# Kernel tuning notes

Hardware: AMD Instinct MI355X
Metric: run time of the kernel (lower is better)

The kernel has to match this reference:

```python
import jax, jax.numpy as jnp
import numpy as np

D = 1024       # d_model
S = 32         # n_slots
EMA = 0.05     # slot_ema (alpha)
RSCALE = 1.0   # read_logit_scale
LN_EPS = 1e-5


def setup_inputs() -> dict:
    key = jax.random.key(0)
    ks = jax.random.split(key, 6)
    B, T = 2, 2048
    h = jax.random.normal(ks[0], (B, T, D), jnp.float32)
    # init_batched_memory_state: small random slots
    state0 = jax.random.normal(ks[1], (B, S, D), jnp.float32) * 0.01
    # xavier_uniform for (out=D, in=D) Linear weights, zero bias
    bound = float(np.sqrt(6.0 / (D + D)))
    Wq = jax.random.uniform(ks[2], (D, D), jnp.float32, -bound, bound)
    Wv = jax.random.uniform(ks[3], (D, D), jnp.float32, -bound, bound)
    bq = jnp.zeros((D,), jnp.float32)
    bv = jnp.zeros((D,), jnp.float32)
    ln_gamma = jnp.ones((D,), jnp.float32)
    ln_beta = jnp.zeros((D,), jnp.float32)
    return {"h": h, "state0": state0, "ln_gamma": ln_gamma, "ln_beta": ln_beta,
            "Wq": Wq, "bq": bq, "Wv": Wv, "bv": bv, "chunk_size": 128}


def _layer_norm(x, gamma, beta):
    mu = jnp.mean(x, axis=-1, keepdims=True)
    var = jnp.mean(jnp.square(x - mu), axis=-1, keepdims=True)
    return (x - mu) * jax.lax.rsqrt(var + LN_EPS) * gamma + beta


def reference(h, state0, ln_gamma, ln_beta, Wq, bq, Wv, bv, chunk_size):
    """write_parallel (soft-routed EMA prefix-scan write) followed by
    read_parallel (per-token softmax slot attention). Returns (ctx, final_state)."""
    B, T, d = h.shape
    alpha = EMA
    a = 1.0 - alpha
    h_norm = _layer_norm(h, ln_gamma, ln_beta)                  # (B,T,d)
    v = h_norm @ Wv.T + bv                                      # value_proj
    q = h_norm @ Wq.T + bq                                      # query_proj
    scale = RSCALE * d ** (-0.5)
    # routing weights from queries vs initial state (breaks seq dependency)
    scores = jnp.einsum('btd,bsd->bts', q, state0) * scale       # (B,T,S)
    w = jax.nn.softmax(scores, axis=-1)
    u = alpha * w[..., None] * v[:, :, None, :]                  # (B,T,S,d)

    n_chunks = T // chunk_size
    Cn = chunk_size
    u_chunks = u.reshape(B, n_chunks, Cn, S, d).transpose(1, 0, 2, 3, 4)
    t_idx = jnp.arange(Cn, dtype=h.dtype)
    decay = a ** t_idx                                           # (Cn,)
    inv_decay = 1.0 / jnp.clip(decay, 1e-30)
    t1_decay = a ** (t_idx + 1.0)

    def step(state, u_c):  # state (B,S,d), u_c (B,Cn,S,d)
        cs = jnp.cumsum(u_c * inv_decay[None, :, None, None], axis=1)
        chunk_states = (decay[None, :, None, None] * cs
                        + t1_decay[None, :, None, None] * state[:, None])
        return chunk_states[:, -1], chunk_states

    final_state, states = jax.lax.scan(step, state0, u_chunks)
    states = states.transpose(1, 0, 2, 3, 4).reshape(B, T, S, d)  # (B,T,S,d)

    # read_parallel: softmax slot attention per token against its own state
    scores_r = jnp.einsum('btd,btsd->bts', q, states) * scale
    attn = jax.nn.softmax(scores_r, axis=-1)
    ctx = jnp.einsum('bts,btsd->btd', attn, states)               # (B,T,d)
    return ctx, final_state
```

## Files before the change

### kernel.cpp

```cpp
#include <hip/hip_runtime.h>

#define Bn 2
#define Tn 2048
#define Dn 1024
#define Sn 32
#define CH 64
#define NCH 32
#define ALPHA 0.05f
#define Adec 0.95f
#define SCALE 0.03125f

typedef __attribute__((ext_vector_type(8))) __bf16 bf16x8;
typedef __attribute__((ext_vector_type(4))) __bf16 bf16x4;
typedef __attribute__((ext_vector_type(4))) float f32x4;

__device__ __forceinline__ void async_copy16(const void* g, void* l) {
  __builtin_amdgcn_global_load_lds(
      (const __attribute__((address_space(1))) unsigned int*)g,
      (__attribute__((address_space(3))) unsigned int*)l, 16, 0, 0);
}

__device__ __forceinline__ bool is_bf16(const void* gam) {
  return ((const unsigned short*)gam)[0] == 0x3F80u;
}

#define W8 (Dn * Dn / 8)
#define S8 (Bn * Sn * Dn / 8)
#define LNB (Bn * Tn)
__global__ __launch_bounds__(256) void prep_k(
    const void* __restrict__ hp, const void* __restrict__ gp, const void* __restrict__ bp,
    const void* __restrict__ Wq, const void* __restrict__ Wv, const void* __restrict__ s0,
    __bf16* __restrict__ hn, __bf16* __restrict__ Wqb, __bf16* __restrict__ Wvb,
    __bf16* __restrict__ s0b) {
  bool isb = is_bf16(gp);
  int tid = threadIdx.x;
  if (blockIdx.x >= LNB) {
    int g = (blockIdx.x - LNB) * 256 + tid;
    const void* src; __bf16* dst; int off;
    if (g < W8)            { src = Wq; dst = Wqb; off = g; }
    else if (g < 2 * W8)   { src = Wv; dst = Wvb; off = g - W8; }
    else                   { src = s0; dst = s0b; off = g - 2 * W8; }
    if (isb) {
      *(bf16x8*)&dst[(size_t)off * 8] = ((const bf16x8*)src)[off];
    } else {
      const float* s = (const float*)src + (size_t)off * 8;
      f32x4 a = *(const f32x4*)s, b = *(const f32x4*)(s + 4);
      bf16x8 t;
      t[0] = (__bf16)a[0]; t[1] = (__bf16)a[1]; t[2] = (__bf16)a[2]; t[3] = (__bf16)a[3];
      t[4] = (__bf16)b[0]; t[5] = (__bf16)b[1]; t[6] = (__bf16)b[2]; t[7] = (__bf16)b[3];
      *(bf16x8*)&dst[(size_t)off * 8] = t;
    }
    return;
  }
  int row = blockIdx.x;
  float x0, x1, x2, x3;
  if (isb) {
    const __bf16* x = (const __bf16*)hp + (size_t)row * Dn;
    bf16x4 xv = *(const bf16x4*)&x[tid * 4];
    x0 = (float)xv[0]; x1 = (float)xv[1]; x2 = (float)xv[2]; x3 = (float)xv[3];
  } else {
    const float* x = (const float*)hp + (size_t)row * Dn;
    f32x4 xv = *(const f32x4*)&x[tid * 4];
    x0 = xv[0]; x1 = xv[1]; x2 = xv[2]; x3 = xv[3];
  }
  float s  = x0 + x1 + x2 + x3;
  float s2 = x0*x0 + x1*x1 + x2*x2 + x3*x3;
  #pragma unroll
  for (int m = 32; m >= 1; m >>= 1) { s += __shfl_xor(s, m); s2 += __shfl_xor(s2, m); }
  __shared__ float red[8];
  int wave = tid >> 6, lane = tid & 63;
  if (lane == 0) { red[wave] = s; red[4 + wave] = s2; }
  __syncthreads();
  s  = red[0] + red[1] + red[2] + red[3];
  s2 = red[4] + red[5] + red[6] + red[7];
  float mu  = s * (1.0f / Dn);
  float var = s2 * (1.0f / Dn) - mu * mu;
  float rs  = rsqrtf(var + 1e-5f);
  float g0, g1, g2, g3, be0, be1, be2, be3;
  if (isb) {
    bf16x4 gv = *(const bf16x4*)&((const __bf16*)gp)[tid * 4];
    bf16x4 bv = *(const bf16x4*)&((const __bf16*)bp)[tid * 4];
    g0 = (float)gv[0]; g1 = (float)gv[1]; g2 = (float)gv[2]; g3 = (float)gv[3];
    be0 = (float)bv[0]; be1 = (float)bv[1]; be2 = (float)bv[2]; be3 = (float)bv[3];
  } else {
    f32x4 gv = *(const f32x4*)&((const float*)gp)[tid * 4];
    f32x4 bv = *(const f32x4*)&((const float*)bp)[tid * 4];
    g0 = gv[0]; g1 = gv[1]; g2 = gv[2]; g3 = gv[3];
    be0 = bv[0]; be1 = bv[1]; be2 = bv[2]; be3 = bv[3];
  }
  bf16x4 o;
  o[0] = (__bf16)((x0 - mu) * rs * g0 + be0);
  o[1] = (__bf16)((x1 - mu) * rs * g1 + be1);
  o[2] = (__bf16)((x2 - mu) * rs * g2 + be2);
  o[3] = (__bf16)((x3 - mu) * rs * g3 + be3);
  *(bf16x4*)&hn[(size_t)row * Dn + tid * 4] = o;
}

__global__ __launch_bounds__(256) void gemm_qv_k(
    const __bf16* __restrict__ A,
    const __bf16* __restrict__ Wqb, const void* __restrict__ bqp,
    const __bf16* __restrict__ Wvb, const void* __restrict__ bvp,
    const void* __restrict__ gam,
    __bf16* __restrict__ Qo, __bf16* __restrict__ Vo) {
  const int K = Dn, N = Dn;
  bool isb = is_bf16(gam);
  int mt = blockIdx.x & 63;
  int nt = blockIdx.x >> 6;
  int m0 = mt * 64, n0 = nt * 128;
  __shared__ alignas(16) __bf16 lA[64 * 64];
  __shared__ alignas(16) __bf16 lBq[128 * 64];
  __shared__ alignas(16) __bf16 lBv[128 * 64];
  int tid = threadIdx.x, lane = tid & 63, wave = tid >> 6;
  int isv = wave >> 1, wn = (wave & 1) * 64;
  int lm = lane & 15, q8 = (lane >> 4) * 8;
  f32x4 zero4 = {0.f, 0.f, 0.f, 0.f};
  f32x4 acc[4][4];
  #pragma unroll
  for (int i = 0; i < 4; ++i)
    #pragma unroll
    for (int j = 0; j < 4; ++j) acc[i][j] = zero4;

  for (int k0 = 0; k0 < K; k0 += 64) {
    __syncthreads();
    #pragma unroll
    for (int r = 0; r < 2; ++r) {
      int idx = r * 256 + tid;
      int row = idx >> 3, c8 = (idx & 7) * 8;
      async_copy16(&A[(size_t)(m0 + row) * K + k0 + c8], &lA[idx * 8]);
    }
    #pragma unroll
    for (int r = 0; r < 4; ++r) {
      int idx = r * 256 + tid;
      int row = idx >> 3, c8 = (idx & 7) * 8;
      async_copy16(&Wqb[(size_t)(n0 + row) * K + k0 + c8], &lBq[idx * 8]);
      async_copy16(&Wvb[(size_t)(n0 + row) * K + k0 + c8], &lBv[idx * 8]);
    }
    __syncthreads();
    const __bf16* lB = isv ? lBv : lBq;
    #pragma unroll
    for (int kk = 0; kk < 64; kk += 32) {
      bf16x8 af[4], bfr[4];
      #pragma unroll
      for (int i = 0; i < 4; ++i) {
        af[i]  = *(const bf16x8*)&lA[(i * 16 + lm) * 64 + kk + q8];
        bfr[i] = *(const bf16x8*)&lB[(wn + i * 16 + lm) * 64 + kk + q8];
      }
      #pragma unroll
      for (int i = 0; i < 4; ++i)
        #pragma unroll
        for (int j = 0; j < 4; ++j)
          acc[i][j] = __builtin_amdgcn_mfma_f32_16x16x32_bf16(af[i], bfr[j], acc[i][j], 0, 0, 0);
    }
  }
  const void* biasp = isv ? bvp : bqp;
  __bf16* O = isv ? Vo : Qo;
  int r4 = (lane >> 4) * 4;
  #pragma unroll
  for (int j = 0; j < 4; ++j) {
    int colN = n0 + wn + j * 16 + lm;
    float bb = isb ? (float)((const __bf16*)biasp)[colN] : ((const float*)biasp)[colN];
    #pragma unroll
    for (int i = 0; i < 4; ++i) {
      int row0 = m0 + i * 16 + r4;
      #pragma unroll
      for (int r = 0; r < 4; ++r)
        O[(size_t)(row0 + r) * N + colN] = (__bf16)(acc[i][j][r] + bb);
    }
  }
}

__global__ __launch_bounds__(256) void router_k(const __bf16* __restrict__ qb,
    const __bf16* __restrict__ s0b, float* __restrict__ wbuf) {
  int tokBase = blockIdx.x * 16;
  int b = tokBase >> 11;
  int tid = threadIdx.x, lane = tid & 63, wave = tid >> 6;
  int lm = lane & 15, q8 = (lane >> 4) * 8;
  const __bf16* qrow = qb + (size_t)(tokBase + lm) * Dn + q8;
  const __bf16* s0r  = s0b + ((size_t)b * Sn + lm) * Dn + q8;
  const __bf16* s1r  = s0r + (size_t)16 * Dn;
  f32x4 zero4 = {0.f, 0.f, 0.f, 0.f};
  f32x4 acc0 = zero4, acc1 = zero4;
  #pragma unroll
  for (int ks = 0; ks < 8; ++ks) {
    int k0 = wave * 256 + ks * 32;
    bf16x8 af = *(const bf16x8*)&qrow[k0];
    bf16x8 b0 = *(const bf16x8*)&s0r[k0];
    bf16x8 b1 = *(const bf16x8*)&s1r[k0];
    acc0 = __builtin_amdgcn_mfma_f32_16x16x32_bf16(af, b0, acc0, 0, 0, 0);
    acc1 = __builtin_amdgcn_mfma_f32_16x16x32_bf16(af, b1, acc1, 0, 0, 0);
  }
  __shared__ float red[4][16][33];
  int r4 = (lane >> 4) * 4;
  #pragma unroll
  for (int r = 0; r < 4; ++r) {
    red[wave][r4 + r][lm]      = acc0[r];
    red[wave][r4 + r][lm + 16] = acc1[r];
  }
  __syncthreads();
  int t = tid >> 4, s = tid & 15;
  float sc0 = (red[0][t][s]      + red[1][t][s])      + (red[2][t][s]      + red[3][t][s]);
  float sc1 = (red[0][t][s + 16] + red[1][t][s + 16]) + (red[2][t][s + 16] + red[3][t][s + 16]);
  sc0 *= SCALE; sc1 *= SCALE;
  float mx = fmaxf(sc0, sc1);
  #pragma unroll
  for (int m = 8; m >= 1; m >>= 1) mx = fmaxf(mx, __shfl_xor(mx, m));
  float e0 = __expf(sc0 - mx), e1 = __expf(sc1 - mx);
  float su = e0 + e1;
  #pragma unroll
  for (int m = 8; m >= 1; m >>= 1) su += __shfl_xor(su, m);
  float inv = 1.f / su;
  wbuf[(size_t)(tokBase + t) * Sn + s]      = e0 * inv;
  wbuf[(size_t)(tokBase + t) * Sn + s + 16] = e1 * inv;
}

__global__ __launch_bounds__(256) void contrib_k(const __bf16* __restrict__ v,
    const float* __restrict__ wbuf, float* __restrict__ contrib) {
  int blk = blockIdx.x;
  int bc = blk >> 2, dq = blk & 3;
  int b = bc >> 5, c = bc & 31;
  int tokBase = b * Tn + c * CH;
  int d0 = dq * 256;
  __shared__ alignas(16) float coef[CH * Sn];
  __shared__ float dp[CH];
  int tid = threadIdx.x;
  if (tid < CH) dp[tid] = powf(Adec, (float)(CH - 1 - tid));
  __syncthreads();
  for (int i = tid; i < CH * Sn; i += 256) {
    int j = i >> 5;
    coef[i] = ALPHA * dp[j] * wbuf[(size_t)tokBase * Sn + i];
  }
  __syncthreads();
  int st = tid >> 6;
  int dg = tid & 63;
  int d4 = d0 + dg * 4;
  int sb = st * 8;
  f32x4 zero4 = {0.f, 0.f, 0.f, 0.f};
  f32x4 acc[8];
  #pragma unroll
  for (int i = 0; i < 8; ++i) acc[i] = zero4;
  for (int j = 0; j < CH; ++j) {
    bf16x4 vv = *(const bf16x4*)&v[(size_t)(tokBase + j) * Dn + d4];
    f32x4 vf = {(float)vv[0], (float)vv[1], (float)vv[2], (float)vv[3]};
    f32x4 c0 = *(const f32x4*)&coef[j * Sn + sb];
    f32x4 c1 = *(const f32x4*)&coef[j * Sn + sb + 4];
    acc[0] += vf * c0[0]; acc[1] += vf * c0[1]; acc[2] += vf * c0[2]; acc[3] += vf * c0[3];
    acc[4] += vf * c1[0]; acc[5] += vf * c1[1]; acc[6] += vf * c1[2]; acc[7] += vf * c1[3];
  }
  float* outp = contrib + (size_t)bc * Sn * Dn;
  #pragma unroll
  for (int i = 0; i < 8; ++i)
    *(f32x4*)&outp[(size_t)(sb + i) * Dn + d4] = acc[i];
}

__global__ __launch_bounds__(256) void scan_k(const void* __restrict__ s0p,
    const float* __restrict__ contrib, const void* __restrict__ gam,
    __bf16* __restrict__ S0b, void* __restrict__ outp) {
  int idx = blockIdx.x * 256 + threadIdx.x;
  bool isb = is_bf16(gam);
  int b = idx >> 15, sd = idx & 32767;
  float val = isb ? (float)((const __bf16*)s0p)[idx] : ((const float*)s0p)[idx];
  const float aC = powf(Adec, (float)CH);
  float cv[NCH];
  #pragma unroll
  for (int c = 0; c < NCH; ++c)
    cv[c] = contrib[((size_t)(b * NCH + c) << 15) + sd];
  #pragma unroll
  for (int c = 0; c < NCH; ++c) {
    S0b[((size_t)(b * NCH + c) << 15) + sd] = (__bf16)val;
    val = aC * val + cv[c];
  }
  size_t fsbase = (size_t)Bn * Tn * Dn;
  if (isb) ((__bf16*)outp)[fsbase + idx] = (__bf16)val;
  else     ((float*)outp)[fsbase + idx] = val;
}

__global__ __launch_bounds__(256) void attn_k(
    const __bf16* __restrict__ q, const __bf16* __restrict__ v,
    const float* __restrict__ wbuf, const __bf16* __restrict__ S0b,
    float* __restrict__ Pbuf, float* __restrict__ A2buf) {
  int bc = blockIdx.x;
  int b = bc >> 5, c = bc & 31;
  int tokBase = b * Tn + c * CH;
  const __bf16* S0c = S0b + (size_t)bc * Sn * Dn;

  __shared__ alignas(16) __bf16 lQ[CH * Dn];
  __shared__ alignas(16) char ovl[28 * 1024];
  __bf16* lV = (__bf16*)ovl;
  __bf16* lS = (__bf16*)(ovl + 8192);
  __bf16* lM  = (__bf16*)ovl;
  __bf16* lW  = (__bf16*)(ovl + 9216);
  __bf16* lWt = (__bf16*)(ovl + 14336);
  __bf16* lAt = (__bf16*)(ovl + 18944);
  float*  dp  = (float*)(ovl + 24064);

  int tid = threadIdx.x, lane = tid & 63, wave = tid >> 6;
  int lm = lane & 15, q8 = (lane >> 4) * 8;
  int r4 = (lane >> 4) * 4;
  f32x4 zero4 = {0.f, 0.f, 0.f, 0.f};
  f32x4 aQV[4], aQS[2];
  #pragma unroll
  for (int i = 0; i < 4; ++i) aQV[i] = zero4;
  aQS[0] = zero4; aQS[1] = zero4;

  #pragma unroll
  for (int r = 0; r < 32; ++r) {
    int idx = r * 256 + tid;
    async_copy16(&q[(size_t)(tokBase + (idx >> 7)) * Dn + (idx & 127) * 8], &lQ[idx * 8]);
  }
  if (tid < CH + 1) dp[tid] = powf(Adec, (float)tid);

  for (int k0 = 0; k0 < Dn; k0 += 64) {
    {
      int idx = tid;
      int row = idx >> 3, c8 = (idx & 7) * 8;
      async_copy16(&v[(size_t)(tokBase + row) * Dn + k0 + c8], &lV[idx * 8]);
      async_copy16(&v[(size_t)(tokBase + 32 + row) * Dn + k0 + c8], &lV[(256 + idx) * 8]);
    }
    async_copy16(&S0c[(size_t)(tid >> 3) * Dn + k0 + (tid & 7) * 8], &lS[tid * 8]);
    __syncthreads();
    #pragma unroll
    for (int kk = 0; kk < 64; kk += 32) {
      bf16x8 af = *(const bf16x8*)&lQ[(wave * 16 + lm) * Dn + k0 + kk + q8];
      #pragma unroll
      for (int j = 0; j < 4; ++j) {
        bf16x8 bb = *(const bf16x8*)&lV[(j * 16 + lm) * 64 + kk + q8];
        aQV[j] = __builtin_amdgcn_mfma_f32_16x16x32_bf16(af, bb, aQV[j], 0, 0, 0);
      }
      #pragma unroll
      for (int j = 0; j < 2; ++j) {
        bf16x8 bb = *(const bf16x8*)&lS[(j * 16 + lm) * 64 + kk + q8];
        aQS[j] = __builtin_amdgcn_mfma_f32_16x16x32_bf16(af, bb, aQS[j], 0, 0, 0);
      }
    }
    __syncthreads();
  }

  for (int i = tid; i < CH * Sn; i += 256) {
    int j = i >> 5, s = i & 31;
    __bf16 wb = (__bf16)wbuf[(size_t)tokBase * Sn + i];
    lW[j * 40 + s] = wb;
    lWt[s * 72 + j] = wb;
  }
  #pragma unroll
  for (int jt = 0; jt < 4; ++jt)
    #pragma unroll
    for (int r = 0; r < 4; ++r) {
      int t = wave * 16 + r4 + r, j = jt * 16 + lm;
      float f = (j <= t) ? ALPHA * dp[t - j] : 0.0f;
      lM[t * 72 + j] = (__bf16)(aQV[jt][r] * f);
    }
  __syncthreads();

  f32x4 sc[2]; sc[0] = zero4; sc[1] = zero4;
  #pragma unroll
  for (int kt = 0; kt < 2; ++kt) {
    bf16x8 am = *(const bf16x8*)&lM[(wave * 16 + lm) * 72 + kt * 32 + q8];
    #pragma unroll
    for (int st = 0; st < 2; ++st) {
      bf16x8 bb = *(const bf16x8*)&lWt[(st * 16 + lm) * 72 + kt * 32 + q8];
      sc[st] = __builtin_amdgcn_mfma_f32_16x16x32_bf16(am, bb, sc[st], 0, 0, 0);
    }
  }
  float at0[4], at1[4];
  #pragma unroll
  for (int r = 0; r < 4; ++r) {
    int t = wave * 16 + r4 + r;
    float aQ = dp[t + 1];
    float s0v = SCALE * (aQ * aQS[0][r] + sc[0][r]);
    float s1v = SCALE * (aQ * aQS[1][r] + sc[1][r]);
    float mx = fmaxf(s0v, s1v);
    #pragma unroll
    for (int m = 8; m >= 1; m >>= 1) mx = fmaxf(mx, __shfl_xor(mx, m));
    float e0 = __expf(s0v - mx), e1 = __expf(s1v - mx);
    float su = e0 + e1;
    #pragma unroll
    for (int m = 8; m >= 1; m >>= 1) su += __shfl_xor(su, m);
    float inv = 1.f / su;
    at0[r] = e0 * inv; at1[r] = e1 * inv;
    A2buf[(size_t)bc * CH * Sn + t * Sn + lm]      = aQ * at0[r];
    A2buf[(size_t)bc * CH * Sn + t * Sn + 16 + lm] = aQ * at1[r];
    lAt[t * 40 + lm]      = (__bf16)at0[r];
    lAt[t * 40 + 16 + lm] = (__bf16)at1[r];
  }
  bf16x8 aa = *(const bf16x8*)&lAt[(wave * 16 + lm) * 40 + q8];
  #pragma unroll
  for (int jt = 0; jt < 4; ++jt) {
    bf16x8 bb = *(const bf16x8*)&lW[(jt * 16 + lm) * 40 + q8];
    f32x4 pj = __builtin_amdgcn_mfma_f32_16x16x32_bf16(aa, bb, zero4, 0, 0, 0);
    #pragma unroll
    for (int r = 0; r < 4; ++r) {
      int t = wave * 16 + r4 + r, j = jt * 16 + lm;
      float val = (j <= t) ? ALPHA * dp[t - j] * pj[r] : 0.0f;
      Pbuf[(size_t)bc * CH * CH + t * CH + j] = val;
    }
  }
}

__global__ __launch_bounds__(256) void ctx_k(const __bf16* __restrict__ v,
    const __bf16* __restrict__ S0b, const float* __restrict__ Pbuf,
    const float* __restrict__ A2buf, const void* __restrict__ gam,
    void* __restrict__ ctxp) {
  int blk = blockIdx.x;
  int bc = blk >> 3, dt = blk & 7;
  int b = bc >> 5, c = bc & 31;
  int tokBase = b * Tn + c * CH;
  int d0 = dt * 128;
  bool isb = is_bf16(gam);
  __shared__ alignas(16) float lP[CH * CH];
  __shared__ alignas(16) float lA2[CH * Sn];
  __shared__ alignas(16) __bf16 lV[CH * 128];
  __shared__ alignas(16) __bf16 lS[Sn * 128];
  int tid = threadIdx.x;
  {
    const f32x4* src = (const f32x4*)(Pbuf + (size_t)bc * CH * CH);
    f32x4* dst = (f32x4*)lP;
    for (int i = tid; i < CH * CH / 4; i += 256) dst[i] = src[i];
    const f32x4* src2 = (const f32x4*)(A2buf + (size_t)bc * CH * Sn);
    f32x4* dst2 = (f32x4*)lA2;
    for (int i = tid; i < CH * Sn / 4; i += 256) dst2[i] = src2[i];
    for (int i = tid; i < CH * 128 / 8; i += 256) {
      int j = i >> 4, dd = (i & 15) * 8;
      *(bf16x8*)&lV[j * 128 + dd] = *(const bf16x8*)&v[(size_t)(tokBase + j) * Dn + d0 + dd];
    }
    for (int i = tid; i < Sn * 128 / 8; i += 256) {
      int s = i >> 4, dd = (i & 15) * 8;
      *(bf16x8*)&lS[s * 128 + dd] = *(const bf16x8*)&S0b[((size_t)bc * Sn + s) * Dn + d0 + dd];
    }
  }
  __syncthreads();
  int tt = tid >> 5, dg = tid & 31;
  int t0 = tt * 8, d4 = dg * 4;
  f32x4 zero4 = {0.f, 0.f, 0.f, 0.f};
  f32x4 acc[8];
  #pragma unroll
  for (int i = 0; i < 8; ++i) acc[i] = zero4;
  for (int j4 = 0; j4 < CH; j4 += 4) {
    f32x4 vf[4];
    #pragma unroll
    for (int k = 0; k < 4; ++k) {
      bf16x4 vv = *(const bf16x4*)&lV[(j4 + k) * 128 + d4];
      vf[k] = f32x4{(float)vv[0], (float)vv[1], (float)vv[2], (float)vv[3]};
    }
    #pragma unroll
    for (int i = 0; i < 8; ++i) {
      f32x4 pr = *(const f32x4*)&lP[(t0 + i) * CH + j4];
      acc[i] += vf[0] * pr[0]; acc[i] += vf[1] * pr[1];
      acc[i] += vf[2] * pr[2]; acc[i] += vf[3] * pr[3];
    }
  }
  for (int s4 = 0; s4 < Sn; s4 += 4) {
    f32x4 sf[4];
    #pragma unroll
    for (int k = 0; k < 4; ++k) {
      bf16x4 sv = *(const bf16x4*)&lS[(s4 + k) * 128 + d4];
      sf[k] = f32x4{(float)sv[0], (float)sv[1], (float)sv[2], (float)sv[3]};
    }
    #pragma unroll
    for (int i = 0; i < 8; ++i) {
      f32x4 ar = *(const f32x4*)&lA2[(t0 + i) * Sn + s4];
      acc[i] += sf[0] * ar[0]; acc[i] += sf[1] * ar[1];
      acc[i] += sf[2] * ar[2]; acc[i] += sf[3] * ar[3];
    }
  }
  if (isb) {
    __bf16* ctx = (__bf16*)ctxp;
    #pragma unroll
    for (int i = 0; i < 8; ++i) {
      bf16x4 o;
      o[0] = (__bf16)acc[i][0]; o[1] = (__bf16)acc[i][1];
      o[2] = (__bf16)acc[i][2]; o[3] = (__bf16)acc[i][3];
      *(bf16x4*)&ctx[(size_t)(tokBase + t0 + i) * Dn + d0 + d4] = o;
    }
  } else {
    float* ctx = (float*)ctxp;
    #pragma unroll
    for (int i = 0; i < 8; ++i)
      *(f32x4*)&ctx[(size_t)(tokBase + t0 + i) * Dn + d0 + d4] = acc[i];
  }
}

extern "C" void kernel_launch(void* const* d_in, const int* in_sizes, int n_in,
                              void* d_out, int out_size, void* d_ws, size_t ws_size,
                              hipStream_t stream) {
  (void)in_sizes; (void)n_in; (void)out_size; (void)ws_size;
  const void* h      = d_in[0];
  const void* state0 = d_in[1];
  const void* gam    = d_in[2];
  const void* bet    = d_in[3];
  const void* Wq     = d_in[4];
  const void* bq     = d_in[5];
  const void* Wv     = d_in[6];
  const void* bv     = d_in[7];

  char* ws = (char*)d_ws;
  __bf16* hn      = (__bf16*)(ws);
  __bf16* qb      = (__bf16*)(ws + (8u << 20));
  __bf16* vb      = (__bf16*)(ws + (16u << 20));
  float*  wbuf    = (float*)(ws + (24u << 20));
  float*  contrib = (float*)(ws + (25u << 20));
  __bf16* S0b     = (__bf16*)(ws + (34u << 20));
  float*  Pbuf    = (float*)(ws + (43u << 20));
  float*  A2buf   = (float*)(ws + (45u << 20));
  __bf16* Wqb     = (__bf16*)(ws + (47u << 20));
  __bf16* Wvb     = (__bf16*)(ws + (49u << 20));
  __bf16* s0b     = (__bf16*)(ws + (51u << 20));

  int convBlocks = (2 * W8 + S8) / 256;
  prep_k<<<LNB + convBlocks, 256, 0, stream>>>(h, gam, bet, Wq, Wv, state0,
                                               hn, Wqb, Wvb, s0b);
  gemm_qv_k<<<512, 256, 0, stream>>>(hn, Wqb, bq, Wvb, bv, gam, qb, vb);
  router_k<<<Bn * Tn / 16, 256, 0, stream>>>(qb, s0b, wbuf);
  contrib_k<<<Bn * NCH * 4, 256, 0, stream>>>(vb, wbuf, contrib);
  scan_k<<<Bn * Sn * Dn / 256, 256, 0, stream>>>(state0, contrib, gam, S0b, d_out);
  attn_k<<<Bn * NCH, 256, 0, stream>>>(qb, vb, wbuf, S0b, Pbuf, A2buf);
  ctx_k<<<Bn * NCH * 8, 256, 0, stream>>>(vb, S0b, Pbuf, A2buf, gam, d_out);
}
```

Before: 177.8 us.

## Compute ctx_k output with bf16 MFMA over fused P|A2 and V|S0 operands

After: 169.4 us. 4.7% less time.

```diff
diff --git a/kernel.cpp b/kernel.cpp
--- a/kernel.cpp
+++ b/kernel.cpp
@@ -396,6 +396,7 @@
   }
 }
 
+#define KP 104
 __global__ __launch_bounds__(256) void ctx_k(const __bf16* __restrict__ v,
     const __bf16* __restrict__ S0b, const float* __restrict__ Pbuf,
     const float* __restrict__ A2buf, const void* __restrict__ gam,
@@ -406,76 +407,108 @@
   int tokBase = b * Tn + c * CH;
   int d0 = dt * 128;
   bool isb = is_bf16(gam);
-  __shared__ alignas(16) float lP[CH * CH];
-  __shared__ alignas(16) float lA2[CH * Sn];
   __shared__ alignas(16) __bf16 lV[CH * 128];
-  __shared__ alignas(16) __bf16 lS[Sn * 128];
-  int tid = threadIdx.x;
-  {
-    const f32x4* src = (const f32x4*)(Pbuf + (size_t)bc * CH * CH);
-    f32x4* dst = (f32x4*)lP;
-    for (int i = tid; i < CH * CH / 4; i += 256) dst[i] = src[i];
-    const f32x4* src2 = (const f32x4*)(A2buf + (size_t)bc * CH * Sn);
-    f32x4* dst2 = (f32x4*)lA2;
-    for (int i = tid; i < CH * Sn / 4; i += 256) dst2[i] = src2[i];
-    for (int i = tid; i < CH * 128 / 8; i += 256) {
-      int j = i >> 4, dd = (i & 15) * 8;
-      *(bf16x8*)&lV[j * 128 + dd] = *(const bf16x8*)&v[(size_t)(tokBase + j) * Dn + d0 + dd];
-    }
-    for (int i = tid; i < Sn * 128 / 8; i += 256) {
-      int s = i >> 4, dd = (i & 15) * 8;
-      *(bf16x8*)&lS[s * 128 + dd] = *(const bf16x8*)&S0b[((size_t)bc * Sn + s) * Dn + d0 + dd];
-    }
-  }
-  __syncthreads();
-  int tt = tid >> 5, dg = tid & 31;
-  int t0 = tt * 8, d4 = dg * 4;
+  __shared__ alignas(16) __bf16 lS2[Sn * 128];
+  __shared__ alignas(16) __bf16 lA[CH * KP];
+  __shared__ alignas(16) __bf16 lBt[128 * KP];
+  int tid = threadIdx.x, lane = tid & 63, wave = tid >> 6;
+  int lm = lane & 15, q8 = (lane >> 4) * 8, r4 = (lane >> 4) * 4;
+
+  #pragma unroll
+  for (int r = 0; r < 4; ++r) {
+    int idx = r * 256 + tid;
+    int j = idx >> 4, cc = idx & 15;
+    bf16x8 gv = *(const bf16x8*)&v[(size_t)(tokBase + j) * Dn + d0 + cc * 8];
+    *(bf16x8*)&lV[j * 128 + (cc ^ (j >> 3)) * 8] = gv;
+  }
+  #pragma unroll
+  for (int r = 0; r < 2; ++r) {
+    int idx = r * 256 + tid;
+    int s = idx >> 4, cc = idx & 15;
+    bf16x8 gv = *(const bf16x8*)&S0b[((size_t)bc * Sn + s) * Dn + d0 + cc * 8];
+    *(bf16x8*)&lS2[s * 128 + (cc ^ (s >> 3)) * 8] = gv;
+  }
+  #pragma unroll
+  for (int r = 0; r < 4; ++r) {
+    int idx = r * 256 + tid;
+    int t = idx >> 4, j4 = (idx & 15) * 4;
+    f32x4 pv = *(const f32x4*)&Pbuf[(size_t)bc * CH * CH + t * CH + j4];
+    bf16x4 pb;
+    pb[0] = (__bf16)pv[0]; pb[1] = (__bf16)pv[1];
+    pb[2] = (__bf16)pv[2]; pb[3] = (__bf16)pv[3];
+    *(bf16x4*)&lA[t * KP + j4] = pb;
+  }
+  #pragma unroll
+  for (int r = 0; r < 2; ++r) {
+    int idx = r * 256 + tid;
+    int t = idx >> 3, s4 = (idx & 7) * 4;
+    f32x4 av = *(const f32x4*)&A2buf[(size_t)bc * CH * Sn + t * Sn + s4];
+    bf16x4 ab;
+    ab[0] = (__bf16)av[0]; ab[1] = (__bf16)av[1];
+    ab[2] = (__bf16)av[2]; ab[3] = (__bf16)av[3];
+    *(bf16x4*)&lA[t * KP + 64 + s4] = ab;
+  }
+  __syncthreads();
+
+  #pragma unroll
+  for (int r = 0; r < 4; ++r) {
+    int idx = r * 256 + tid;
+    int n = idx >> 3, j8 = idx & 7;
+    bf16x8 pk;
+    #pragma unroll
+    for (int e = 0; e < 8; ++e) {
+      int j = j8 * 8 + e;
+      pk[e] = lV[j * 128 + (((n >> 3) ^ (j >> 3)) * 8) + (n & 7)];
+    }
+    *(bf16x8*)&lBt[n * KP + j8 * 8] = pk;
+  }
+  #pragma unroll
+  for (int r = 0; r < 2; ++r) {
+    int idx = r * 256 + tid;
+    int n = idx >> 2, s8 = idx & 3;
+    bf16x8 pk;
+    #pragma unroll
+    for (int e = 0; e < 8; ++e) {
+      int s = s8 * 8 + e;
+      pk[e] = lS2[s * 128 + (((n >> 3) ^ (s >> 3)) * 8) + (n & 7)];
+    }
+    *(bf16x8*)&lBt[n * KP + 64 + s8 * 8] = pk;
+  }
+  __syncthreads();
+
   f32x4 zero4 = {0.f, 0.f, 0.f, 0.f};
-  f32x4 acc[8];
-  #pragma unroll
-  for (int i = 0; i < 8; ++i) acc[i] = zero4;
-  for (int j4 = 0; j4 < CH; j4 += 4) {
-    f32x4 vf[4];
-    #pragma unroll
-    for (int k = 0; k < 4; ++k) {
-      bf16x4 vv = *(const bf16x4*)&lV[(j4 + k) * 128 + d4];
-      vf[k] = f32x4{(float)vv[0], (float)vv[1], (float)vv[2], (float)vv[3]};
-    }
-    #pragma unroll
-    for (int i = 0; i < 8; ++i) {
-      f32x4 pr = *(const f32x4*)&lP[(t0 + i) * CH + j4];
-      acc[i] += vf[0] * pr[0]; acc[i] += vf[1] * pr[1];
-      acc[i] += vf[2] * pr[2]; acc[i] += vf[3] * pr[3];
-    }
-  }
-  for (int s4 = 0; s4 < Sn; s4 += 4) {
-    f32x4 sf[4];
-    #pragma unroll
-    for (int k = 0; k < 4; ++k) {
-      bf16x4 sv = *(const bf16x4*)&lS[(s4 + k) * 128 + d4];
-      sf[k] = f32x4{(float)sv[0], (float)sv[1], (float)sv[2], (float)sv[3]};
-    }
-    #pragma unroll
-    for (int i = 0; i < 8; ++i) {
-      f32x4 ar = *(const f32x4*)&lA2[(t0 + i) * Sn + s4];
-      acc[i] += sf[0] * ar[0]; acc[i] += sf[1] * ar[1];
-      acc[i] += sf[2] * ar[2]; acc[i] += sf[3] * ar[3];
-    }
-  }
-  if (isb) {
-    __bf16* ctx = (__bf16*)ctxp;
-    #pragma unroll
-    for (int i = 0; i < 8; ++i) {
-      bf16x4 o;
-      o[0] = (__bf16)acc[i][0]; o[1] = (__bf16)acc[i][1];
-      o[2] = (__bf16)acc[i][2]; o[3] = (__bf16)acc[i][3];
-      *(bf16x4*)&ctx[(size_t)(tokBase + t0 + i) * Dn + d0 + d4] = o;
-    }
-  } else {
-    float* ctx = (float*)ctxp;
-    #pragma unroll
-    for (int i = 0; i < 8; ++i)
-      *(f32x4*)&ctx[(size_t)(tokBase + t0 + i) * Dn + d0 + d4] = acc[i];
+  f32x4 acc[2][4];
+  #pragma unroll
+  for (int i = 0; i < 2; ++i)
+    #pragma unroll
+    for (int m = 0; m < 4; ++m) acc[i][m] = zero4;
+  #pragma unroll
+  for (int kt = 0; kt < 3; ++kt) {
+    bf16x8 af[4];
+    #pragma unroll
+    for (int m = 0; m < 4; ++m)
+      af[m] = *(const bf16x8*)&lA[(m * 16 + lm) * KP + kt * 32 + q8];
+    #pragma unroll
+    for (int nt2 = 0; nt2 < 2; ++nt2) {
+      bf16x8 bf = *(const bf16x8*)&lBt[((2 * wave + nt2) * 16 + lm) * KP + kt * 32 + q8];
+      #pragma unroll
+      for (int m = 0; m < 4; ++m)
+        acc[nt2][m] = __builtin_amdgcn_mfma_f32_16x16x32_bf16(af[m], bf, acc[nt2][m], 0, 0, 0);
+    }
+  }
+  #pragma unroll
+  for (int nt2 = 0; nt2 < 2; ++nt2) {
+    int d = d0 + (2 * wave + nt2) * 16 + lm;
+    #pragma unroll
+    for (int m = 0; m < 4; ++m) {
+      int t0 = m * 16 + r4;
+      #pragma unroll
+      for (int rr = 0; rr < 4; ++rr) {
+        size_t off = (size_t)(tokBase + t0 + rr) * Dn + d;
+        if (isb) ((__bf16*)ctxp)[off] = (__bf16)acc[nt2][m][rr];
+        else     ((float*)ctxp)[off]  = acc[nt2][m][rr];
+      }
+    }
   }
 }
 
```
